# Optimization experiments

Hardware: AMD Instinct MI355X
Metric: run time of the kernel (lower is better)

Reference implementation:

```python
import jax, jax.numpy as jnp
import numpy as np

N_NODES, N_EDGES, HIDDEN, N_GRAPHS, TARGET, DEPTH, N_FOURIER = 20000, 320000, 128, 64, 32, 4, 4


def setup_inputs() -> dict:
    key = jax.random.key(0)
    ks = iter(jax.random.split(key, 48))
    H, L = HIDDEN, DEPTH

    def nrm(shape, fan):
        return jax.random.normal(next(ks), shape, jnp.float32) / np.sqrt(fan)

    inp = {}
    inp["x"] = jnp.zeros((N_NODES, 9), jnp.int32)  # only N is used (use_node_features=False)
    src = jax.random.randint(next(ks), (N_EDGES,), 0, N_NODES, dtype=jnp.int32)
    dst = jax.random.randint(next(ks), (N_EDGES,), 0, N_NODES, dtype=jnp.int32)
    inp["edge_index"] = jnp.stack([src, dst])  # row0 = x_j (source), row1 = x_i (target)
    inp["edge_attr"] = jax.random.uniform(next(ks), (N_EDGES,), jnp.float32) * 5.0  # distances
    inp["batch"] = ((jnp.arange(N_NODES) * N_GRAPHS) // N_NODES).astype(jnp.int32)  # sorted, all graphs non-empty

    ein = 2 * N_FOURIER + 1
    inp["node_embedding"] = jax.random.normal(next(ks), (H,), jnp.float32)
    inp["edge_W"] = nrm((ein, H), ein); inp["edge_b"] = jnp.zeros((H,), jnp.float32)
    # stacked per-mp-layer params (scanned over)
    inp["msg_W1"] = nrm((L, 3 * H, H), 3 * H); inp["msg_b1"] = jnp.zeros((L, H), jnp.float32)
    inp["msg_W2"] = nrm((L, H, H), H);        inp["msg_b2"] = jnp.zeros((L, H), jnp.float32)
    inp["soft_W"] = nrm((L, H, 1), H);        inp["soft_b"] = jnp.zeros((L, 1), jnp.float32)
    inp["upd_W1"] = nrm((L, H, H), H);        inp["upd_b1"] = jnp.zeros((L, H), jnp.float32)
    inp["upd_W2"] = nrm((L, H, H), H);        inp["upd_b2"] = jnp.zeros((L, H), jnp.float32)
    # node-wise output MLP (2 layers, last_activation=None)
    inp["no_W1"] = nrm((H, H), H); inp["no_b1"] = jnp.zeros((H,), jnp.float32)
    inp["no_W2"] = nrm((H, H), H); inp["no_b2"] = jnp.zeros((H,), jnp.float32)
    # readout MLP: in = 3*H (mean, sum, max), hidden = H, out = TARGET
    inp["out_W1"] = nrm((3 * H, H), 3 * H); inp["out_b1"] = jnp.zeros((H,), jnp.float32)
    inp["out_W2"] = nrm((H, TARGET), H);    inp["out_b2"] = jnp.zeros((TARGET,), jnp.float32)
    return inp


def _forward(x, edge_index, edge_attr, batch, node_embedding, edge_W, edge_b,
             msg_W1, msg_b1, msg_W2, msg_b2, soft_W, soft_b,
             upd_W1, upd_b1, upd_W2, upd_b2,
             no_W1, no_b1, no_W2, no_b2, out_W1, out_b1, out_W2, out_b2):
    N = x.shape[0]
    silu = jax.nn.silu
    h = jnp.broadcast_to(node_embedding, (N, node_embedding.shape[0]))

    # fourier_encode_dist: [E] -> [E, 2*F+1]
    scales = 2.0 ** jnp.arange(N_FOURIER, dtype=edge_attr.dtype)
    d = edge_attr[:, None] / scales
    e = jnp.concatenate([jnp.sin(d), jnp.cos(d), edge_attr[:, None]], axis=-1)
    # edge_input MLP (layers=1, last_activation=SiLU) followed by extra F.silu in forward
    e = silu(silu(e @ edge_W + edge_b))

    src, dst = edge_index[0], edge_index[1]  # x_j gathers src, x_i gathers dst

    def layer(carry, p):
        h, e = carry
        W1, b1, W2, b2, sW, sb, uW1, ub1, uW2, ub2 = p
        m_in = jnp.concatenate([h[src], h[dst], e], axis=-1)  # [x_j, x_i, edge_attr]
        m = silu(silu(m_in @ W1 + b1) @ W2 + b2)              # message MLP, last_activation=SiLU
        e = e + m                                             # in-place edge_attr += message
        w = jax.nn.sigmoid(m @ sW + sb)                       # soft edge gate
        agg = jax.ops.segment_sum(m * w, dst, num_segments=N) # aggr='sum' to targets
        hn = silu((agg + h) @ uW1 + ub1) @ uW2 + ub2          # update MLP, last_activation=None
        return (h + hn, e), None

    (h, e), _ = jax.lax.scan(layer, (h, e),
                             (msg_W1, msg_b1, msg_W2, msg_b2, soft_W, soft_b,
                              upd_W1, upd_b1, upd_W2, upd_b2))

    h = silu(h @ no_W1 + no_b1) @ no_W2 + no_b2  # node-wise output network

    G = N_GRAPHS
    s = jax.ops.segment_sum(h, batch, num_segments=G)
    cnt = jax.ops.segment_sum(jnp.ones((N, 1), h.dtype), batch, num_segments=G)
    mean = s / jnp.maximum(cnt, 1.0)
    mx = jax.ops.segment_max(h, batch, num_segments=G)
    readout = jnp.concatenate([mean, s, mx], axis=-1)  # aggregators = [mean, sum, max]
    return jax.nn.relu(readout @ out_W1 + out_b1) @ out_W2 + out_b2


def reference(x, edge_index, edge_attr, batch, node_embedding, edge_W, edge_b,
              msg_W1, msg_b1, msg_W2, msg_b2, soft_W, soft_b,
              upd_W1, upd_b1, upd_W2, upd_b2,
              no_W1, no_b1, no_W2, no_b2, out_W1, out_b1, out_W2, out_b2):
    return _forward(x, edge_index, edge_attr, batch, node_embedding, edge_W, edge_b,
                    msg_W1, msg_b1, msg_W2, msg_b2, soft_W, soft_b,
                    upd_W1, upd_b1, upd_W2, upd_b2,
                    no_W1, no_b1, no_W2, no_b2, out_W1, out_b1, out_W2, out_b2)
```

## Files before the change

### kernel.cpp

```cpp
#include <hip/hip_runtime.h>

#define N_NODES 20000
#define N_EDGES 320000
#define HID 128
#define NG 64
#define TGT 32
#define DEPTHL 4
#define NTILES 20000
#define MSG_WAVES 15
#define MSG_SLOTS (256 * MSG_WAVES)

typedef __attribute__((ext_vector_type(8))) short s16x8;
typedef __attribute__((ext_vector_type(4))) short s16x4;
typedef __attribute__((ext_vector_type(4))) float f32x4;

__device__ __forceinline__ unsigned short f2b(float f) {
  unsigned u = __builtin_bit_cast(unsigned, f);
  u = (u + 0x7FFFu + ((u >> 16) & 1u)) >> 16;
  return (unsigned short)u;
}
__device__ __forceinline__ float b2f(unsigned short s) {
  return __builtin_bit_cast(float, ((unsigned)s) << 16);
}
__device__ __forceinline__ float silu_f(float x) {
  return x * __builtin_amdgcn_rcpf(1.f + __expf(-x));
}
__device__ __forceinline__ float sigmoid_f(float x) {
  return __builtin_amdgcn_rcpf(1.f + __expf(-x));
}

__device__ __forceinline__ unsigned fkey(float f) {
  unsigned u = __builtin_bit_cast(unsigned, f);
  return (u & 0x80000000u) ? ~u : (u | 0x80000000u);
}
__device__ __forceinline__ float unkey(unsigned k) {
  unsigned u = (k & 0x80000000u) ? (k ^ 0x80000000u) : ~k;
  return __builtin_bit_cast(float, u);
}

__device__ __forceinline__ f32x4 mfma16(s16x8 a, s16x8 b, f32x4 c) {
  return __builtin_amdgcn_mfma_f32_16x16x32_bf16(a, b, c, 0, 0, 0);
}

__device__ __forceinline__ void lds_fence() {
  asm volatile("s_waitcnt lgkmcnt(0)" ::: "memory");
  __builtin_amdgcn_sched_barrier(0);
}

__device__ __forceinline__ s16x8 pack8(float4 a, float4 b) {
  s16x8 p;
  p[0]=(short)f2b(a.x); p[1]=(short)f2b(a.y); p[2]=(short)f2b(a.z); p[3]=(short)f2b(a.w);
  p[4]=(short)f2b(b.x); p[5]=(short)f2b(b.y); p[6]=(short)f2b(b.z); p[7]=(short)f2b(b.w);
  return p;
}

__global__ void pack_weights(const float* __restrict__ mW1, const float* __restrict__ mW2,
                             const float* __restrict__ uW1, const float* __restrict__ uW2,
                             const float* __restrict__ nW1, const float* __restrict__ nW2,
                             short* __restrict__ pMsg,
                             short* __restrict__ puW1, short* __restrict__ puW2,
                             short* __restrict__ pnW1, short* __restrict__ pnW2) {
  int i = blockIdx.x * 256 + threadIdx.x;
  const float* src; short* dst; int K, r;
  if (i < 196608)      { int l = i/49152; r = i % 49152; src = mW1 + l*49152; dst = pMsg + l*65536 + r;        K = 384; }
  else if (i < 262144) { int q = i - 196608; int l = q/16384; r = q % 16384; src = mW2 + l*16384; dst = pMsg + l*65536 + 49152 + r; K = 128; }
  else if (i < 327680) { int q = i - 262144; src = uW1 + (q/16384)*16384; dst = puW1 + q; r = q % 16384; K = 128; }
  else if (i < 393216) { int q = i - 327680; src = uW2 + (q/16384)*16384; dst = puW2 + q; r = q % 16384; K = 128; }
  else if (i < 409600) { int q = i - 393216; src = nW1; dst = pnW1 + q; r = q; K = 128; }
  else if (i < 425984) { int q = i - 409600; src = nW2; dst = pnW2 + q; r = q; K = 128; }
  else return;
  int j = r & 7, lane = (r >> 3) & 63, q2 = r >> 9;
  int KT = K >> 5;
  int kt = q2 % KT, ct = q2 / KT;
  int k = kt*32 + ((lane >> 4) << 3) + j;
  int col = ct*16 + (lane & 15);
  dst[0] = (short)f2b(src[k*HID + col]);
}

__global__ void sort_init(int* __restrict__ hist, int* __restrict__ cursor) {
  int i = blockIdx.x * 256 + threadIdx.x;
  if (i < N_NODES) { hist[i] = 0; cursor[i] = 0; }
}

__global__ void hist_kernel(const int* __restrict__ dst, int* __restrict__ hist) {
  int e = blockIdx.x * 256 + threadIdx.x;
  if (e < N_EDGES) atomicAdd(&hist[dst[e]], 1);
}

__global__ __launch_bounds__(1024) void scan_kernel(const int* __restrict__ hist,
                                                    int* __restrict__ offs) {
  __shared__ int part[1024];
  int t = threadIdx.x;
  int base = t * 20;
  int loc[20];
  int s = 0;
#pragma unroll
  for (int i = 0; i < 20; ++i) {
    loc[i] = s;
    int n = base + i;
    s += (n < N_NODES ? hist[n] : 0);
  }
  part[t] = s;
  __syncthreads();
  for (int st = 1; st < 1024; st <<= 1) {
    int v = (t >= st) ? part[t - st] : 0;
    __syncthreads();
    part[t] += v;
    __syncthreads();
  }
  int pre = (t > 0) ? part[t - 1] : 0;
#pragma unroll
  for (int i = 0; i < 20; ++i) {
    int n = base + i;
    if (n < N_NODES) offs[n] = pre + loc[i];
  }
}

__global__ void scatter_kernel(const int* __restrict__ src, const int* __restrict__ dst,
                               const float* __restrict__ ea, const int* __restrict__ offs,
                               int* __restrict__ cursor,
                               unsigned short* __restrict__ ssrc,
                               unsigned short* __restrict__ sdst,
                               float* __restrict__ sea) {
  int e = blockIdx.x * 256 + threadIdx.x;
  if (e >= N_EDGES) return;
  int d = dst[e];
  int pos = offs[d] + atomicAdd(&cursor[d], 1);
  ssrc[pos] = (unsigned short)src[e];
  sdst[pos] = (unsigned short)d;
  sea[pos] = ea[e];
}

__global__ void edge_init(const float* __restrict__ sea, const float* __restrict__ eW,
                          const float* __restrict__ eb, unsigned short* __restrict__ e) {
  __shared__ float feat[2][9];
  int t = threadIdx.x;
  int le = t >> 7, c = t & 127;
  int edge = blockIdx.x * 2 + le;
  if (c < 9) {
    float d = sea[edge];
    float sc = (float)(1 << (c & 3));
    float v;
    if (c < 4) v = sinf(d / sc);
    else if (c < 8) v = cosf(d / sc);
    else v = d;
    feat[le][c] = v;
  }
  __syncthreads();
  float acc = eb[c];
#pragma unroll
  for (int j = 0; j < 9; ++j) acc += feat[le][j] * eW[j*HID + c];
  acc = silu_f(silu_f(acc));
  e[edge*HID + c] = f2b(acc);
}

__global__ void init_h(float* __restrict__ h, const float* __restrict__ ne,
                       float* __restrict__ agg, unsigned short* __restrict__ hb) {
  int i = blockIdx.x * 256 + threadIdx.x;
  if (i < N_NODES * HID) {
    float v = ne[i & 127];
    h[i] = v; hb[i] = f2b(v); agg[i] = 0.f;
  }
}

__global__ void init_read(float* __restrict__ s, float* __restrict__ cnt, unsigned* __restrict__ mx) {
  int i = blockIdx.x * 256 + threadIdx.x;
  if (i < NG * HID) { s[i] = 0.f; mx[i] = 0x007FFFFFu; }
  if (i < NG) cnt[i] = 0.f;
}

__global__ __launch_bounds__(960) void msg_kernel(
    const unsigned short* __restrict__ hb, unsigned short* __restrict__ e,
    const unsigned short* __restrict__ ssrc, const unsigned short* __restrict__ sdst,
    const short* __restrict__ Wp, const float* __restrict__ b1,
    const float* __restrict__ b2,
    const float* __restrict__ sW, const float* __restrict__ sbp,
    float* __restrict__ agg) {
  __shared__ __align__(16) short smem[80896];
  short* sW1 = smem;
  short* sW2 = smem + 49152;
  int t = threadIdx.x;
  int wv = t >> 6, lane = t & 63;
  int l15 = lane & 15, hi = lane >> 4;
  short* myt1 = smem + 65536 + wv * 1024;

  {
    const s16x8* Wg = (const s16x8*)Wp;
    s16x8* Wl = (s16x8*)smem;
    for (int i = t; i < 8192; i += 960) Wl[i] = Wg[i];
  }
  __syncthreads();

  float sb_v = sbp[0];
  int slot = blockIdx.x * MSG_WAVES + wv;

#pragma unroll 1
  for (int it = 0; it < 6; ++it) {
    int tile = slot + MSG_SLOTS * it;
    if (tile >= NTILES) break;
    int edge = tile * 16 + l15;
    int si = ssrc[edge];
    int d  = sdst[edge];

    s16x8 bfrag[12];
#pragma unroll
    for (int kt = 0; kt < 4; ++kt)
      bfrag[kt] = *(const s16x8*)(hb + si*HID + kt*32 + hi*8);
#pragma unroll
    for (int kt = 0; kt < 4; ++kt)
      bfrag[4+kt] = *(const s16x8*)(hb + d*HID + kt*32 + hi*8);
#pragma unroll
    for (int kt = 0; kt < 4; ++kt)
      bfrag[8+kt] = *(const s16x8*)(e + (size_t)edge*HID + kt*32 + hi*8);

    f32x4 acc1[8];
#pragma unroll
    for (int ct = 0; ct < 8; ++ct) acc1[ct] = f32x4{0.f, 0.f, 0.f, 0.f};
#pragma unroll
    for (int kt = 0; kt < 12; ++kt) {
#pragma unroll
      for (int ct = 0; ct < 8; ++ct) {
        s16x8 afr = *(const s16x8*)&sW1[((ct*12 + kt)*64 + lane)*8];
        acc1[ct] = mfma16(afr, bfrag[kt], acc1[ct]);
      }
    }

    uint2 eold[8];
#pragma unroll
    for (int ct = 0; ct < 8; ++ct)
      eold[ct] = *(const uint2*)(e + (size_t)edge*HID + ct*16 + hi*4);

    f32x4 acc2[8];
#pragma unroll
    for (int ct = 0; ct < 8; ++ct) acc2[ct] = f32x4{0.f, 0.f, 0.f, 0.f};
#pragma unroll
    for (int p = 0; p < 2; ++p) {
#pragma unroll
      for (int c4 = 0; c4 < 4; ++c4) {
        int ct = 4*p + c4;
        f32x4 bias = *(const f32x4*)(b1 + ct*16 + hi*4);
        s16x4 pk4;
#pragma unroll
        for (int r = 0; r < 4; ++r) pk4[r] = (short)f2b(silu_f(acc1[ct][r] + bias[r]));
        *(s16x4*)&myt1[((2*c4 + (hi >> 1))*16 + l15)*8 + (hi & 1)*4] = pk4;
      }
      lds_fence();
#pragma unroll
      for (int k2 = 0; k2 < 2; ++k2) {
        int kt = 2*p + k2;
        s16x8 bfr = *(const s16x8*)&myt1[((k2*4 + hi)*16 + l15)*8];
#pragma unroll
        for (int ct = 0; ct < 8; ++ct) {
          s16x8 afr = *(const s16x8*)&sW2[((ct*4 + kt)*64 + lane)*8];
          acc2[ct] = mfma16(afr, bfr, acc2[ct]);
        }
      }
      lds_fence();
    }

    uint2 mpk[8];
    float wpart = 0.f;
#pragma unroll
    for (int ct = 0; ct < 8; ++ct) {
      f32x4 bias = *(const f32x4*)(b2 + ct*16 + hi*4);
      f32x4 swv  = *(const f32x4*)(sW + ct*16 + hi*4);
      f32x4 mv;
#pragma unroll
      for (int r = 0; r < 4; ++r) {
        mv[r] = silu_f(acc2[ct][r] + bias[r]);
        wpart += mv[r] * swv[r];
      }
      mpk[ct].x = (unsigned)f2b(mv[0]) | ((unsigned)f2b(mv[1]) << 16);
      mpk[ct].y = (unsigned)f2b(mv[2]) | ((unsigned)f2b(mv[3]) << 16);
    }
    wpart += __shfl_xor(wpart, 16);
    wpart += __shfl_xor(wpart, 32);
    float wg = sigmoid_f(wpart + sb_v);

    int pd = __shfl_up(d, 1, 16);
    bool head = (l15 == 0) || (pd != d);
    int okbits = 0;
#pragma unroll
    for (int i = 0; i < 4; ++i) {
      int off = 1 << i;
      int nd = __shfl_down(d, off, 16);
      if ((l15 + off < 16) && (nd == d)) okbits |= (1 << i);
    }
    float* aggrow = agg + d*HID;

#pragma unroll
    for (int ct = 0; ct < 8; ++ct) {
      float m0 = b2f((unsigned short)(mpk[ct].x & 0xFFFFu));
      float m1 = b2f((unsigned short)(mpk[ct].x >> 16));
      float m2 = b2f((unsigned short)(mpk[ct].y & 0xFFFFu));
      float m3 = b2f((unsigned short)(mpk[ct].y >> 16));

      uint2 cur = eold[ct];
      float f0 = b2f((unsigned short)(cur.x & 0xFFFFu)) + m0;
      float f1 = b2f((unsigned short)(cur.x >> 16))     + m1;
      float f2v = b2f((unsigned short)(cur.y & 0xFFFFu)) + m2;
      float f3 = b2f((unsigned short)(cur.y >> 16))     + m3;
      uint2 nw;
      nw.x = (unsigned)f2b(f0)  | ((unsigned)f2b(f1) << 16);
      nw.y = (unsigned)f2b(f2v) | ((unsigned)f2b(f3) << 16);
      *(uint2*)(e + (size_t)edge*HID + ct*16 + hi*4) = nw;

      f32x4 v;
      v[0] = m0 * wg; v[1] = m1 * wg; v[2] = m2 * wg; v[3] = m3 * wg;
#pragma unroll
      for (int i = 0; i < 4; ++i) {
        int off = 1 << i;
        bool ok = (okbits >> i) & 1;
#pragma unroll
        for (int r = 0; r < 4; ++r) {
          float nv = __shfl_down(v[r], off, 16);
          if (ok) v[r] += nv;
        }
      }
      if (head) {
        float* ap = aggrow + ct*16 + hi*4;
        atomicAdd(ap + 0, v[0]);
        atomicAdd(ap + 1, v[1]);
        atomicAdd(ap + 2, v[2]);
        atomicAdd(ap + 3, v[3]);
      }
    }
  }
}

template<int MODE>
__global__ __launch_bounds__(512) void node_kernel(
    float* __restrict__ h, float* __restrict__ agg,
    const short* __restrict__ W1p, const float* __restrict__ b1,
    const short* __restrict__ W2p, const float* __restrict__ b2,
    float* __restrict__ out, unsigned short* __restrict__ hb) {
  __shared__ __align__(16) short t1f[8][2048];
  int t = threadIdx.x;
  int wv = t >> 6, lane = t & 63;
  int l15 = lane & 15, hi = lane >> 4;
  int node = blockIdx.x * 128 + wv * 16 + l15;
  bool valid = node < N_NODES;
  int nodec = valid ? node : (N_NODES - 1);

  s16x8 bfrag[4];
#pragma unroll
  for (int kt = 0; kt < 4; ++kt) {
    const float* hp = h + nodec*HID + kt*32 + hi*8;
    float4 v0 = *(const float4*)hp;
    float4 v1 = *(const float4*)(hp + 4);
    if (MODE == 0) {
      float* ap = agg + nodec*HID + kt*32 + hi*8;
      float4 a0 = *(const float4*)ap;
      float4 a1 = *(const float4*)(ap + 4);
      v0.x += a0.x; v0.y += a0.y; v0.z += a0.z; v0.w += a0.w;
      v1.x += a1.x; v1.y += a1.y; v1.z += a1.z; v1.w += a1.w;
      if (valid) {
        float4 z = {0.f, 0.f, 0.f, 0.f};
        *(float4*)ap = z;
        *(float4*)(ap + 4) = z;
      }
    }
    bfrag[kt] = pack8(v0, v1);
  }

  f32x4 acc1[8];
#pragma unroll
  for (int ct = 0; ct < 8; ++ct) acc1[ct] = f32x4{0.f, 0.f, 0.f, 0.f};
#pragma unroll
  for (int kt = 0; kt < 4; ++kt) {
#pragma unroll
    for (int ct = 0; ct < 8; ++ct) {
      s16x8 afr = *(const s16x8*)(W1p + ((ct*4 + kt)*64 + lane)*8);
      acc1[ct] = mfma16(afr, bfrag[kt], acc1[ct]);
    }
  }
  short* myt1 = &t1f[wv][0];
#pragma unroll
  for (int ct = 0; ct < 8; ++ct) {
    f32x4 bias = *(const f32x4*)(b1 + ct*16 + hi*4);
    s16x4 pk4;
#pragma unroll
    for (int r = 0; r < 4; ++r) pk4[r] = (short)f2b(silu_f(acc1[ct][r] + bias[r]));
    *(s16x4*)&myt1[((2*ct + (hi >> 1))*16 + l15)*8 + (hi & 1)*4] = pk4;
  }
  lds_fence();

  f32x4 acc2[8];
#pragma unroll
  for (int ct = 0; ct < 8; ++ct) acc2[ct] = f32x4{0.f, 0.f, 0.f, 0.f};
#pragma unroll
  for (int kt = 0; kt < 4; ++kt) {
    s16x8 bfr = *(const s16x8*)&myt1[((kt*4 + hi)*16 + l15)*8];
#pragma unroll
    for (int ct = 0; ct < 8; ++ct) {
      s16x8 afr = *(const s16x8*)(W2p + ((ct*4 + kt)*64 + lane)*8);
      acc2[ct] = mfma16(afr, bfr, acc2[ct]);
    }
  }
  if (valid) {
#pragma unroll
    for (int ct = 0; ct < 8; ++ct) {
      f32x4 bias = *(const f32x4*)(b2 + ct*16 + hi*4);
      float* op = (MODE == 0 ? h : out) + node*HID + ct*16 + hi*4;
      float4 res;
      if (MODE == 0) {
        float4 cur = *(const float4*)op;
        res.x = cur.x + acc2[ct][0] + bias[0];
        res.y = cur.y + acc2[ct][1] + bias[1];
        res.z = cur.z + acc2[ct][2] + bias[2];
        res.w = cur.w + acc2[ct][3] + bias[3];
      } else {
        res.x = acc2[ct][0] + bias[0];
        res.y = acc2[ct][1] + bias[1];
        res.z = acc2[ct][2] + bias[2];
        res.w = acc2[ct][3] + bias[3];
      }
      *(float4*)op = res;
      if (MODE == 0) {
        uint2 nb;
        nb.x = (unsigned)f2b(res.x) | ((unsigned)f2b(res.y) << 16);
        nb.y = (unsigned)f2b(res.z) | ((unsigned)f2b(res.w) << 16);
        *(uint2*)(hb + node*HID + ct*16 + hi*4) = nb;
      }
    }
  }
}

__global__ void accum_kernel(const float* __restrict__ h2, const int* __restrict__ batch,
                             float* __restrict__ s, float* __restrict__ cnt,
                             unsigned* __restrict__ mx) {
  int c = threadIdx.x & 127;
  int lr = threadIdx.x >> 7;
  int base = blockIdx.x * 64;
  int cur = -1; float sum = 0.f, mxv = -3.0e38f, count = 0.f;
  for (int i = 0; i < 32; ++i) {
    int node = base + lr + 2 * i;
    if (node >= N_NODES) break;
    int g = batch[node];
    if (g != cur) {
      if (cur >= 0) {
        atomicAdd(&s[cur*HID + c], sum);
        atomicMax(&mx[cur*HID + c], fkey(mxv));
        if (c == 0) atomicAdd(&cnt[cur], count);
      }
      cur = g; sum = 0.f; mxv = -3.0e38f; count = 0.f;
    }
    float v = h2[node*HID + c];
    sum += v; mxv = fmaxf(mxv, v); count += 1.f;
  }
  if (cur >= 0) {
    atomicAdd(&s[cur*HID + c], sum);
    atomicMax(&mx[cur*HID + c], fkey(mxv));
    if (c == 0) atomicAdd(&cnt[cur], count);
  }
}

__global__ void final_kernel(const float* __restrict__ s, const float* __restrict__ cnt,
                             const unsigned* __restrict__ mx,
                             const float* __restrict__ W1, const float* __restrict__ b1,
                             const float* __restrict__ W2, const float* __restrict__ b2,
                             float* __restrict__ out) {
  __shared__ float ro[3 * HID];
  __shared__ float r1[HID];
  int g = blockIdx.x, c = threadIdx.x;
  float sv = s[g*HID + c];
  float cn = cnt[g];
  ro[c] = sv / fmaxf(cn, 1.f);
  ro[HID + c] = sv;
  ro[2*HID + c] = unkey(mx[g*HID + c]);
  __syncthreads();
  float acc = b1[c];
  for (int k = 0; k < 3*HID; ++k) acc += ro[k] * W1[k*HID + c];
  r1[c] = fmaxf(acc, 0.f);
  __syncthreads();
  if (c < TGT) {
    float o = b2[c];
    for (int k = 0; k < HID; ++k) o += r1[k] * W2[k*TGT + c];
    out[g*TGT + c] = o;
  }
}

extern "C" void kernel_launch(void* const* d_in, const int* in_sizes, int n_in,
                              void* d_out, int out_size, void* d_ws, size_t ws_size,
                              hipStream_t stream) {
  const int*   eidx = (const int*)d_in[1];
  const int*   srci = eidx;
  const int*   dsti = eidx + N_EDGES;
  const float* ea   = (const float*)d_in[2];
  const int*   batch= (const int*)d_in[3];
  const float* nemb = (const float*)d_in[4];
  const float* eW   = (const float*)d_in[5];
  const float* eb   = (const float*)d_in[6];
  const float* mW1  = (const float*)d_in[7];
  const float* mb1  = (const float*)d_in[8];
  const float* mW2  = (const float*)d_in[9];
  const float* mb2  = (const float*)d_in[10];
  const float* sW   = (const float*)d_in[11];
  const float* sb   = (const float*)d_in[12];
  const float* uW1  = (const float*)d_in[13];
  const float* ub1  = (const float*)d_in[14];
  const float* uW2  = (const float*)d_in[15];
  const float* ub2  = (const float*)d_in[16];
  const float* nW1  = (const float*)d_in[17];
  const float* nb1  = (const float*)d_in[18];
  const float* nW2  = (const float*)d_in[19];
  const float* nb2  = (const float*)d_in[20];
  const float* oW1  = (const float*)d_in[21];
  const float* ob1  = (const float*)d_in[22];
  const float* oW2  = (const float*)d_in[23];
  const float* ob2  = (const float*)d_in[24];

  char* ws = (char*)d_ws;
  float* sbuf = (float*)(ws + 0);
  float* cnt  = (float*)(ws + 32768);
  unsigned* mx= (unsigned*)(ws + 33024);
  short* pMsg = (short*)(ws + 65792);
  short* puW1 = (short*)(ws + 590080);
  short* puW2 = (short*)(ws + 721152);
  short* pnW1 = (short*)(ws + 852224);
  short* pnW2 = (short*)(ws + 884992);
  int* hist   = (int*)(ws + 917760);
  int* cursor = (int*)(ws + 997760);
  int* offs   = (int*)(ws + 1077760);
  unsigned short* ssrc = (unsigned short*)(ws + 1157760);
  unsigned short* sdst = (unsigned short*)(ws + 1797760);
  float* sea  = (float*)(ws + 2437760);
  unsigned short* e = (unsigned short*)(ws + 3717760);
  float* h    = (float*)(ws + 85637760);
  float* agg  = (float*)(ws + 95877760);
  unsigned short* hb = (unsigned short*)(ws + 106117760);
  float* h2   = agg;

  sort_init<<<(N_NODES + 255) / 256, 256, 0, stream>>>(hist, cursor);
  hist_kernel<<<N_EDGES / 256, 256, 0, stream>>>(dsti, hist);
  scan_kernel<<<1, 1024, 0, stream>>>(hist, offs);
  scatter_kernel<<<N_EDGES / 256, 256, 0, stream>>>(srci, dsti, ea, offs, cursor,
                                                    ssrc, sdst, sea);

  pack_weights<<<1664, 256, 0, stream>>>(mW1, mW2, uW1, uW2, nW1, nW2,
                                         pMsg, puW1, puW2, pnW1, pnW2);
  edge_init<<<N_EDGES / 2, 256, 0, stream>>>(sea, eW, eb, e);
  init_h<<<(N_NODES * HID) / 256, 256, 0, stream>>>(h, nemb, agg, hb);
  init_read<<<33, 256, 0, stream>>>(sbuf, cnt, mx);

  for (int l = 0; l < DEPTHL; ++l) {
    msg_kernel<<<256, 960, 0, stream>>>(hb, e, ssrc, sdst,
        pMsg + l*65536, mb1 + l*HID, mb2 + l*HID,
        sW + l*HID, sb + l, agg);
    node_kernel<0><<<(N_NODES + 127) / 128, 512, 0, stream>>>(h, agg,
        puW1 + l*16384, ub1 + l*HID, puW2 + l*16384, ub2 + l*HID, nullptr, hb);
  }
  node_kernel<1><<<(N_NODES + 127) / 128, 512, 0, stream>>>(h, nullptr,
      pnW1, nb1, pnW2, nb2, h2, nullptr);
  accum_kernel<<<(N_NODES + 63) / 64, 256, 0, stream>>>(h2, batch, sbuf, cnt, mx);
  final_kernel<<<NG, 128, 0, stream>>>(sbuf, cnt, mx, oW1, ob1, oW2, ob2, (float*)d_out);
}
```

Measured before the change: 787.1 us.

## Software-pipeline msg_kernel gathers and shrink block to 12 waves

The message kernel now prefetches the next tile's source/destination indices and bf16 gather fragments (h_src, h_dst, e) into registers while the current tile's first MFMA GEMM runs. This is meant to hide the gather latency behind compute. To leave registers for the doubled fragment buffers, the block shrinks from 15 to 12 waves, with the loop trip count and LDS size adjusted to match. The costs are higher register pressure, fewer waves per CU to hide latency, and more tiles processed serially per wave.

```diff
diff --git a/kernel.cpp b/kernel.cpp
--- a/kernel.cpp
+++ b/kernel.cpp
@@ -7,7 +7,7 @@
 #define TGT 32
 #define DEPTHL 4
 #define NTILES 20000
-#define MSG_WAVES 15
+#define MSG_WAVES 12
 #define MSG_SLOTS (256 * MSG_WAVES)
 
 typedef __attribute__((ext_vector_type(8))) short s16x8;
@@ -169,14 +169,14 @@
   if (i < NG) cnt[i] = 0.f;
 }
 
-__global__ __launch_bounds__(960) void msg_kernel(
+__global__ __launch_bounds__(768) void msg_kernel(
     const unsigned short* __restrict__ hb, unsigned short* __restrict__ e,
     const unsigned short* __restrict__ ssrc, const unsigned short* __restrict__ sdst,
     const short* __restrict__ Wp, const float* __restrict__ b1,
     const float* __restrict__ b2,
     const float* __restrict__ sW, const float* __restrict__ sbp,
     float* __restrict__ agg) {
-  __shared__ __align__(16) short smem[80896];
+  __shared__ __align__(16) short smem[77824];
   short* sW1 = smem;
   short* sW2 = smem + 49152;
   int t = threadIdx.x;
@@ -187,22 +187,20 @@
   {
     const s16x8* Wg = (const s16x8*)Wp;
     s16x8* Wl = (s16x8*)smem;
-    for (int i = t; i < 8192; i += 960) Wl[i] = Wg[i];
+    for (int i = t; i < 8192; i += 768) Wl[i] = Wg[i];
   }
   __syncthreads();
 
   float sb_v = sbp[0];
   int slot = blockIdx.x * MSG_WAVES + wv;
 
-#pragma unroll 1
-  for (int it = 0; it < 6; ++it) {
-    int tile = slot + MSG_SLOTS * it;
-    if (tile >= NTILES) break;
+  int tile = slot;
+  bool valid = tile < NTILES;
+  int si = 0, d = 0;
+  s16x8 bfrag[12];
+  if (valid) {
     int edge = tile * 16 + l15;
-    int si = ssrc[edge];
-    int d  = sdst[edge];
-
-    s16x8 bfrag[12];
+    si = ssrc[edge]; d = sdst[edge];
 #pragma unroll
     for (int kt = 0; kt < 4; ++kt)
       bfrag[kt] = *(const s16x8*)(hb + si*HID + kt*32 + hi*8);
@@ -212,6 +210,18 @@
 #pragma unroll
     for (int kt = 0; kt < 4; ++kt)
       bfrag[8+kt] = *(const s16x8*)(e + (size_t)edge*HID + kt*32 + hi*8);
+  }
+
+#pragma unroll 1
+  for (int it = 0; it < 7; ++it) {
+    if (!valid) break;
+    int edge = tile * 16 + l15;
+
+    int ntile = tile + MSG_SLOTS;
+    bool nvalid = ntile < NTILES;
+    int nsi = 0, nd = 0;
+    int nedge = ntile * 16 + l15;
+    if (nvalid) { nsi = ssrc[nedge]; nd = sdst[nedge]; }
 
     f32x4 acc1[8];
 #pragma unroll
@@ -223,6 +233,19 @@
         s16x8 afr = *(const s16x8*)&sW1[((ct*12 + kt)*64 + lane)*8];
         acc1[ct] = mfma16(afr, bfrag[kt], acc1[ct]);
       }
+    }
+
+    s16x8 bfragN[12];
+    if (nvalid) {
+#pragma unroll
+      for (int kt = 0; kt < 4; ++kt)
+        bfragN[kt] = *(const s16x8*)(hb + nsi*HID + kt*32 + hi*8);
+#pragma unroll
+      for (int kt = 0; kt < 4; ++kt)
+        bfragN[4+kt] = *(const s16x8*)(hb + nd*HID + kt*32 + hi*8);
+#pragma unroll
+      for (int kt = 0; kt < 4; ++kt)
+        bfragN[8+kt] = *(const s16x8*)(e + (size_t)nedge*HID + kt*32 + hi*8);
     }
 
     uint2 eold[8];
@@ -283,8 +306,8 @@
 #pragma unroll
     for (int i = 0; i < 4; ++i) {
       int off = 1 << i;
-      int nd = __shfl_down(d, off, 16);
-      if ((l15 + off < 16) && (nd == d)) okbits |= (1 << i);
+      int nd2 = __shfl_down(d, off, 16);
+      if ((l15 + off < 16) && (nd2 == d)) okbits |= (1 << i);
     }
     float* aggrow = agg + d*HID;
 
@@ -325,6 +348,10 @@
         atomicAdd(ap + 3, v[3]);
       }
     }
+
+    tile = ntile; valid = nvalid; si = nsi; d = nd;
+#pragma unroll
+    for (int j = 0; j < 12; ++j) bfrag[j] = bfragN[j];
   }
 }
 
@@ -544,7 +571,7 @@
   init_read<<<33, 256, 0, stream>>>(sbuf, cnt, mx);
 
   for (int l = 0; l < DEPTHL; ++l) {
-    msg_kernel<<<256, 960, 0, stream>>>(hb, e, ssrc, sdst,
+    msg_kernel<<<256, 768, 0, stream>>>(hb, e, ssrc, sdst,
         pMsg + l*65536, mb1 + l*HID, mb2 + l*HID,
         sW + l*HID, sb + l, agg);
     node_kernel<0><<<(N_NODES + 127) / 128, 512, 0, stream>>>(h, agg,
```

Result: no change. 795.1 us (+1.0%).
